# Performance work log

Hardware: AMD Instinct MI355X
Metric: run time of the kernel (lower is better)

Reference implementation:

```python
import jax, jax.numpy as jnp
import numpy as np

HEADS = 16
DIM_HEAD = 64
SCALE = DIM_HEAD ** -0.5
MASK_NEG = 1000000.0


def setup_inputs() -> dict:
    key = jax.random.key(0)
    ks = jax.random.split(key, 6)
    B, N, M, D = 2, 2048, 2048, 1024
    inner = HEADS * DIM_HEAD  # 1024
    x = jax.random.normal(ks[0], (B, N, D), dtype=jnp.float32)
    context = jax.random.normal(ks[1], (B, M, D), dtype=jnp.float32)
    mask = jax.random.randint(ks[2], (B, N), 0, 2, dtype=jnp.int32)
    Wq = jax.random.normal(ks[3], (D, inner), dtype=jnp.float32) * (D ** -0.5)
    Wkv = jax.random.normal(ks[4], (D, 2 * inner), dtype=jnp.float32) * (D ** -0.5)
    Wout = jax.random.normal(ks[5], (inner, D), dtype=jnp.float32) * (inner ** -0.5)
    bout = jnp.zeros((D,), dtype=jnp.float32)
    return {"x": x, "context": context, "mask": mask,
            "Wq": Wq, "Wkv": Wkv, "Wout": Wout, "bout": bout}


def _split_heads(t):
    # [b, n, (h d)] -> [b, h, n, d]
    b, n, _ = t.shape
    return t.reshape(b, n, HEADS, DIM_HEAD).transpose(0, 2, 1, 3)


def reference(x, context, mask, Wq, Wkv, Wout, bout):
    kv = context @ Wkv                      # [b, m, 2*inner]
    k, v = jnp.split(kv, 2, axis=-1)
    q = x @ Wq                              # [b, n, inner]
    q, k, v = _split_heads(q), _split_heads(k), _split_heads(v)
    dots = jnp.einsum('bhnd,bhmd->bhnm', q, k) * SCALE
    # mask is [b, n]: additive penalty per query row (faithful to source)
    dots = dots - (1.0 - mask.astype(jnp.float32))[:, None, :, None] * MASK_NEG
    attn = jax.nn.softmax(dots, axis=-1)
    out = jnp.einsum('bhnm,bhmd->bhnd', attn, v)  # [b, h, n, d]
    b, h, n, d = out.shape
    out = out.transpose(0, 2, 1, 3).reshape(b, n, h * d)
    return out @ Wout + bout
```

## Files before the change

kernel.cpp:

```cpp
#include <hip/hip_runtime.h>
#include <hip/hip_bf16.h>
#include <math.h>

#define BATCH   2
#define NQ      2048
#define NKV     2048
#define DMODEL  1024
#define HEADS   16
#define INNER   1024
#define KVCOLS  2048

typedef short bf16x8 __attribute__((ext_vector_type(8)));
typedef float f32x4  __attribute__((ext_vector_type(4)));

__device__ __forceinline__ short f2bf(float x) {
    __hip_bfloat16 h = __float2bfloat16(x);
    return *reinterpret_cast<short*>(&h);
}
__device__ __forceinline__ float bf2f(short h) {
    unsigned int u = ((unsigned int)(unsigned short)h) << 16;
    float f;
    __builtin_memcpy(&f, &u, 4);
    return f;
}
__device__ __forceinline__ void gl_lds16(const void* g, void* l) {
    __builtin_amdgcn_global_load_lds(
        (const __attribute__((address_space(1))) unsigned int*)g,
        (__attribute__((address_space(3))) unsigned int*)l, 16, 0, 0);
}
__device__ __forceinline__ int sw(int row, int chunk) {
    return row * 64 + ((chunk ^ (row & 7)) << 3);
}

__device__ __forceinline__ void split_chunk(const float* __restrict__ in,
                                            short* __restrict__ hi,
                                            short* __restrict__ lo, int id)
{
    const int i = (id * 256 + (int)threadIdx.x) * 4;
    float4 v = *(const float4*)(in + i);
    short4 h, l;
    h.x = f2bf(v.x); l.x = f2bf(v.x - bf2f(h.x));
    h.y = f2bf(v.y); l.y = f2bf(v.y - bf2f(h.y));
    h.z = f2bf(v.z); l.z = f2bf(v.z - bf2f(h.z));
    h.w = f2bf(v.w); l.w = f2bf(v.w - bf2f(h.w));
    *(short4*)(hi + i) = h;
    *(short4*)(lo + i) = l;
}

__device__ __forceinline__ void tile_transpose_split(
    const float* __restrict__ W, short* __restrict__ Wth, short* __restrict__ Wtl,
    int Kd, int Nd, int bx, int by, int split)
{
    __shared__ float t[32][33];
    const int lx = threadIdx.x & 31, ly = threadIdx.x >> 5;
    #pragma unroll
    for (int j = 0; j < 4; ++j)
        t[ly + j * 8][lx] = W[(size_t)(by * 32 + ly + j * 8) * Nd + bx * 32 + lx];
    __syncthreads();
    #pragma unroll
    for (int j = 0; j < 4; ++j) {
        const float v = t[lx][ly + j * 8];
        const short h = f2bf(v);
        const size_t idx = (size_t)(bx * 32 + ly + j * 8) * Kd + by * 32 + lx;
        Wth[idx] = h;
        if (split) Wtl[idx] = f2bf(v - bf2f(h));
    }
}

__global__ __launch_bounds__(256)
void prep_all(const float* __restrict__ x, const float* __restrict__ ctx,
              const float* __restrict__ Wq, const float* __restrict__ Wkv,
              const float* __restrict__ Wout,
              short* __restrict__ xh, short* __restrict__ xl,
              short* __restrict__ ch, short* __restrict__ cl,
              short* __restrict__ WqTh, short* __restrict__ WqTl,
              short* __restrict__ WkvTh, short* __restrict__ WkvTl,
              short* __restrict__ WoutT)
{
    const int id = blockIdx.x;
    if (id < 4096) {
        split_chunk(x, xh, xl, id);
    } else if (id < 8192) {
        split_chunk(ctx, ch, cl, id - 4096);
    } else {
        const int r = id - 8192;
        if (r < 1024)
            tile_transpose_split(Wq, WqTh, WqTl, 1024, 1024, r & 31, r >> 5, 1);
        else if (r < 3072)
            tile_transpose_split(Wkv, WkvTh, WkvTl, 1024, 2048, (r - 1024) & 63, (r - 1024) >> 6, 1);
        else
            tile_transpose_split(Wout, WoutT, nullptr, 1024, 1024, (r - 3072) & 31, (r - 3072) >> 5, 0);
    }
}

__global__ __launch_bounds__(256)
void qkv_gemm(const short* __restrict__ xh, const short* __restrict__ xl,
              const short* __restrict__ ch, const short* __restrict__ cl,
              const short* __restrict__ WqTh, const short* __restrict__ WqTl,
              const short* __restrict__ WkvTh, const short* __restrict__ WkvTl,
              short* __restrict__ qhp, short* __restrict__ qlp,
              short* __restrict__ khp, short* __restrict__ klp,
              short* __restrict__ vp)
{
    __shared__ short Ash[128 * 32];
    __shared__ short Asl[128 * 32];
    __shared__ short Bsh[128 * 32];
    __shared__ short Bsl[128 * 32];

    const int tid = threadIdx.x;
    const int z = blockIdx.z;
    const int m0 = blockIdx.y * 128, n0 = blockIdx.x * 128;
    const int w = tid >> 6, ln = tid & 63;
    const int wm = (w & 1) * 64, wn = (w >> 1) * 64;
    const int lr = ln & 15, lq = ln >> 4;
    const int terms = (z == 2) ? 1 : 3;

    const short* Ah  = (z == 0) ? xh : ch;
    const short* Al  = (z == 0) ? xl : cl;
    const short* Bth = (z == 0) ? WqTh : (z == 1 ? WkvTh : WkvTh + (size_t)1024 * 1024);
    const short* Btl = (z == 0) ? WqTl : WkvTl;

    f32x4 acc[4][4];
    #pragma unroll
    for (int mt = 0; mt < 4; ++mt)
        #pragma unroll
        for (int nt = 0; nt < 4; ++nt)
            #pragma unroll
            for (int r = 0; r < 4; ++r) acc[mt][nt][r] = 0.0f;

    for (int k0 = 0; k0 < 1024; k0 += 32) {
        __syncthreads();
        #pragma unroll
        for (int it = 0; it < 2; ++it) {
            const int f = it * 256 + tid;
            const int row = f >> 2, c = f & 3;
            const int cg = c ^ ((row >> 1) & 3);
            const size_t ao = (size_t)(m0 + row) * 1024 + k0 + cg * 8;
            const size_t bo = (size_t)(n0 + row) * 1024 + k0 + cg * 8;
            gl_lds16(Ah  + ao, Ash + f * 8);
            gl_lds16(Bth + bo, Bsh + f * 8);
            if (terms == 3) {
                gl_lds16(Al  + ao, Asl + f * 8);
                gl_lds16(Btl + bo, Bsl + f * 8);
            }
        }
        __syncthreads();

        bf16x8 ah[4], bh[4];
        #pragma unroll
        for (int t = 0; t < 4; ++t) {
            const int ar = wm + t * 16 + lr;
            const int br = wn + t * 16 + lr;
            ah[t] = *(const bf16x8*)(Ash + ar * 32 + ((lq ^ ((ar >> 1) & 3)) << 3));
            bh[t] = *(const bf16x8*)(Bsh + br * 32 + ((lq ^ ((br >> 1) & 3)) << 3));
        }
        #pragma unroll
        for (int mt = 0; mt < 4; ++mt)
            #pragma unroll
            for (int nt = 0; nt < 4; ++nt)
                acc[mt][nt] = __builtin_amdgcn_mfma_f32_16x16x32_bf16(
                    ah[mt], bh[nt], acc[mt][nt], 0, 0, 0);

        if (terms == 3) {
            bf16x8 al[4], bl[4];
            #pragma unroll
            for (int t = 0; t < 4; ++t) {
                const int ar = wm + t * 16 + lr;
                const int br = wn + t * 16 + lr;
                al[t] = *(const bf16x8*)(Asl + ar * 32 + ((lq ^ ((ar >> 1) & 3)) << 3));
                bl[t] = *(const bf16x8*)(Bsl + br * 32 + ((lq ^ ((br >> 1) & 3)) << 3));
            }
            #pragma unroll
            for (int mt = 0; mt < 4; ++mt)
                #pragma unroll
                for (int nt = 0; nt < 4; ++nt) {
                    acc[mt][nt] = __builtin_amdgcn_mfma_f32_16x16x32_bf16(
                        ah[mt], bl[nt], acc[mt][nt], 0, 0, 0);
                    acc[mt][nt] = __builtin_amdgcn_mfma_f32_16x16x32_bf16(
                        al[mt], bh[nt], acc[mt][nt], 0, 0, 0);
                }
        }
    }

    const float scale = (z == 0) ? 0.125f : 1.0f;
    short* Chi = (z == 0) ? qhp : (z == 1 ? khp : vp);
    short* Clo = (z == 0) ? qlp : klp;
    #pragma unroll
    for (int mt = 0; mt < 4; ++mt)
        #pragma unroll
        for (int nt = 0; nt < 4; ++nt)
            #pragma unroll
            for (int r = 0; r < 4; ++r) {
                const int row = m0 + wm + mt * 16 + lq * 4 + r;
                const int col = n0 + wn + nt * 16 + lr;
                const float v = acc[mt][nt][r] * scale;
                const short hh = f2bf(v);
                Chi[(size_t)row * 1024 + col] = hh;
                if (z != 2)
                    Clo[(size_t)row * 1024 + col] = f2bf(v - bf2f(hh));
            }
}

__global__ __launch_bounds__(256)
void gemm_out(const short* __restrict__ A, const short* __restrict__ Bt,
              float* __restrict__ C, int Md, int Nd, int Kd,
              const float* __restrict__ bias)
{
    __shared__ short As[64 * 64];
    __shared__ short Bs[64 * 64];
    const int tid = threadIdx.x;
    const int m0 = blockIdx.y * 64, n0 = blockIdx.x * 64;
    const int w = tid >> 6, ln = tid & 63;
    const int wm = (w & 1) * 32, wn = (w >> 1) * 32;
    const int lr = ln & 15, lq = ln >> 4;

    f32x4 acc[2][2];
    #pragma unroll
    for (int mt = 0; mt < 2; ++mt)
        #pragma unroll
        for (int nt = 0; nt < 2; ++nt)
            #pragma unroll
            for (int r = 0; r < 4; ++r) acc[mt][nt][r] = 0.0f;

    for (int k0 = 0; k0 < Kd; k0 += 64) {
        __syncthreads();
        #pragma unroll
        for (int it = 0; it < 2; ++it) {
            const int f = it * 256 + tid;
            const int row = f >> 3, c8 = f & 7;
            gl_lds16(A  + (size_t)(m0 + row) * Kd + k0 + c8 * 8, As + f * 8);
            gl_lds16(Bt + (size_t)(n0 + row) * Kd + k0 + c8 * 8, Bs + f * 8);
        }
        __syncthreads();
        #pragma unroll
        for (int ks = 0; ks < 2; ++ks) {
            bf16x8 af[2], bfr[2];
            #pragma unroll
            for (int t = 0; t < 2; ++t) {
                af[t]  = *(const bf16x8*)(As + (wm + t * 16 + lr) * 64 + ks * 32 + lq * 8);
                bfr[t] = *(const bf16x8*)(Bs + (wn + t * 16 + lr) * 64 + ks * 32 + lq * 8);
            }
            #pragma unroll
            for (int mt = 0; mt < 2; ++mt)
                #pragma unroll
                for (int nt = 0; nt < 2; ++nt)
                    acc[mt][nt] = __builtin_amdgcn_mfma_f32_16x16x32_bf16(
                        af[mt], bfr[nt], acc[mt][nt], 0, 0, 0);
        }
    }
    #pragma unroll
    for (int mt = 0; mt < 2; ++mt)
        #pragma unroll
        for (int nt = 0; nt < 2; ++nt)
            #pragma unroll
            for (int r = 0; r < 4; ++r) {
                const int row = m0 + wm + mt * 16 + lq * 4 + r;
                const int col = n0 + wn + nt * 16 + lr;
                C[(size_t)row * Nd + col] = acc[mt][nt][r] + bias[col];
            }
}

__global__ __launch_bounds__(512, 4)
void flash_v5(const short* __restrict__ qh, const short* __restrict__ ql,
              const short* __restrict__ kh, const short* __restrict__ kl,
              const short* __restrict__ vp, const int* __restrict__ mask,
              short* __restrict__ aob)
{
    const int qt = blockIdx.x, h = blockIdx.y, b = blockIdx.z;
    const int tid = threadIdx.x;
    const int w = tid >> 6, ln = tid & 63;
    const int lr = ln & 15, lq = ln >> 4;

    __shared__ short Kh[2 * 4096];
    __shared__ short Kl[2 * 4096];
    __shared__ short Vt[2 * 4096];
    __shared__ short Ps[128 * 64];

    const size_t qrow0 = (size_t)(b * NQ + qt * 128);

    bf16x8 aqh[2], aql[2];
    #pragma unroll
    for (int ks = 0; ks < 2; ++ks) {
        const size_t qoff = (qrow0 + w * 16 + lr) * INNER + h * 64 + ks * 32 + lq * 8;
        aqh[ks] = *(const bf16x8*)(qh + qoff);
        aql[ks] = *(const bf16x8*)(ql + qoff);
    }
    float keep[4];
    #pragma unroll
    for (int r = 0; r < 4; ++r)
        keep[r] = (float)mask[b * NQ + qt * 128 + w * 16 + lq * 4 + r];

    const int srow = tid >> 3, sc8 = tid & 7;
    const int kdst = sw(srow, sc8);
    const int kp = tid & 31, dg4 = (tid >> 5) * 4;
    int4 rkh, rkl; int2 rva, rvb;

    {
        const size_t koff = (size_t)(b * NKV + srow) * INNER + h * 64 + sc8 * 8;
        rkh = *(const int4*)(kh + koff);
        rkl = *(const int4*)(kl + koff);
        const short* v0 = vp + (size_t)(b * NKV + 2 * kp) * INNER + h * 64 + dg4;
        rva = *(const int2*)(v0);
        rvb = *(const int2*)(v0 + INNER);
        *(int4*)(Kh + kdst) = rkh;
        *(int4*)(Kl + kdst) = rkl;
        const short* as = (const short*)&rva;
        const short* bs = (const short*)&rvb;
        int* vt32 = (int*)Vt;
        #pragma unroll
        for (int j = 0; j < 4; ++j)
            vt32[(dg4 + j) * 32 + (((kp >> 2) ^ ((dg4 + j) & 7)) << 2) + (kp & 3)] =
                (int)((unsigned short)as[j] | ((unsigned int)(unsigned short)bs[j] << 16));
    }

    float psum[4];
    #pragma unroll
    for (int r = 0; r < 4; ++r) psum[r] = 0.0f;
    f32x4 oacc[4];
    #pragma unroll
    for (int dg = 0; dg < 4; ++dg)
        #pragma unroll
        for (int r = 0; r < 4; ++r) oacc[dg][r] = 0.0f;

    for (int kt = 0; kt < NKV / 64; ++kt) {
        const int cur = kt & 1;
        if (kt < NKV / 64 - 1) {
            const size_t krow0 = (size_t)(b * NKV + (kt + 1) * 64);
            const size_t koff = (krow0 + srow) * INNER + h * 64 + sc8 * 8;
            rkh = *(const int4*)(kh + koff);
            rkl = *(const int4*)(kl + koff);
            const short* v0 = vp + (krow0 + 2 * kp) * INNER + h * 64 + dg4;
            rva = *(const int2*)(v0);
            rvb = *(const int2*)(v0 + INNER);
        }
        __syncthreads();

        const short* KhC = Kh + cur * 4096;
        const short* KlC = Kl + cur * 4096;
        const short* VtC = Vt + cur * 4096;

        f32x4 sacc[4];
        #pragma unroll
        for (int g = 0; g < 4; ++g)
            #pragma unroll
            for (int r = 0; r < 4; ++r) sacc[g][r] = 0.0f;
        #pragma unroll
        for (int ks = 0; ks < 2; ++ks) {
            #pragma unroll
            for (int g = 0; g < 4; ++g) {
                const bf16x8 bkh = *(const bf16x8*)(KhC + sw(g * 16 + lr, ks * 4 + lq));
                const bf16x8 bkl = *(const bf16x8*)(KlC + sw(g * 16 + lr, ks * 4 + lq));
                sacc[g] = __builtin_amdgcn_mfma_f32_16x16x32_bf16(aqh[ks], bkh, sacc[g], 0, 0, 0);
                sacc[g] = __builtin_amdgcn_mfma_f32_16x16x32_bf16(aqh[ks], bkl, sacc[g], 0, 0, 0);
                sacc[g] = __builtin_amdgcn_mfma_f32_16x16x32_bf16(aql[ks], bkh, sacc[g], 0, 0, 0);
            }
        }

        #pragma unroll
        for (int r = 0; r < 4; ++r) {
            const int prow = w * 16 + lq * 4 + r;
            #pragma unroll
            for (int g = 0; g < 4; ++g) {
                float s = sacc[g][r];
                if (keep[r] == 0.0f) s = rintf(s * 16.0f) * 0.0625f;
                const float p = __expf(s);
                psum[r] += p;
                Ps[sw(prow, g * 2 + (lr >> 3)) + (lr & 7)] = f2bf(p);
            }
        }

        #pragma unroll
        for (int ks = 0; ks < 2; ++ks) {
            const bf16x8 ap = *(const bf16x8*)(Ps + sw(w * 16 + lr, ks * 4 + lq));
            #pragma unroll
            for (int dg = 0; dg < 4; ++dg) {
                const bf16x8 bv = *(const bf16x8*)(VtC + sw(dg * 16 + lr, ks * 4 + lq));
                oacc[dg] = __builtin_amdgcn_mfma_f32_16x16x32_bf16(ap, bv, oacc[dg], 0, 0, 0);
            }
        }

        if (kt < NKV / 64 - 1) {
            short* KhN = Kh + (cur ^ 1) * 4096;
            short* KlN = Kl + (cur ^ 1) * 4096;
            *(int4*)(KhN + kdst) = rkh;
            *(int4*)(KlN + kdst) = rkl;
            const short* as = (const short*)&rva;
            const short* bs = (const short*)&rvb;
            int* vt32 = (int*)(Vt + (cur ^ 1) * 4096);
            #pragma unroll
            for (int j = 0; j < 4; ++j)
                vt32[(dg4 + j) * 32 + (((kp >> 2) ^ ((dg4 + j) & 7)) << 2) + (kp & 3)] =
                    (int)((unsigned short)as[j] | ((unsigned int)(unsigned short)bs[j] << 16));
        }
    }

    #pragma unroll
    for (int off = 1; off < 16; off <<= 1)
        #pragma unroll
        for (int r = 0; r < 4; ++r)
            psum[r] += __shfl_xor(psum[r], off, 64);

    #pragma unroll
    for (int dg = 0; dg < 4; ++dg)
        #pragma unroll
        for (int r = 0; r < 4; ++r) {
            const int row = w * 16 + lq * 4 + r;
            aob[(qrow0 + row) * INNER + h * 64 + dg * 16 + lr] =
                f2bf(oacc[dg][r] / psum[r]);
        }
}

extern "C" void kernel_launch(void* const* d_in, const int* in_sizes, int n_in,
                              void* d_out, int out_size, void* d_ws, size_t ws_size,
                              hipStream_t stream)
{
    const float* x    = (const float*)d_in[0];
    const float* ctx  = (const float*)d_in[1];
    const int*   mask = (const int*)d_in[2];
    const float* Wq   = (const float*)d_in[3];
    const float* Wkv  = (const float*)d_in[4];
    const float* Wout = (const float*)d_in[5];
    const float* bout = (const float*)d_in[6];
    float* out = (float*)d_out;

    short* base  = (short*)d_ws;
    short* xh    = base;
    short* xl    = base + (size_t)4 * 1024 * 1024;
    short* aob   = xh;
    short* WqTh  = base + (size_t) 8 * 1024 * 1024;
    short* WqTl  = base + (size_t) 9 * 1024 * 1024;
    short* qhp   = base + (size_t)10 * 1024 * 1024;
    short* qlp   = base + (size_t)14 * 1024 * 1024;
    short* WkvTh = base + (size_t)18 * 1024 * 1024;
    short* WkvTl = base + (size_t)20 * 1024 * 1024;
    short* khp   = base + (size_t)22 * 1024 * 1024;
    short* klp   = base + (size_t)26 * 1024 * 1024;
    short* WoutT = base + (size_t)30 * 1024 * 1024;
    short* ch    = base + (size_t)31 * 1024 * 1024;
    short* cl    = base + (size_t)35 * 1024 * 1024;
    short* vp    = base + (size_t)39 * 1024 * 1024;

    const dim3 blk(256);
    prep_all<<<12288, blk, 0, stream>>>(x, ctx, Wq, Wkv, Wout,
                                        xh, xl, ch, cl,
                                        WqTh, WqTl, WkvTh, WkvTl, WoutT);
    qkv_gemm<<<dim3(8, 32, 3), blk, 0, stream>>>(
        xh, xl, ch, cl, WqTh, WqTl, WkvTh, WkvTl,
        qhp, qlp, khp, klp, vp);
    flash_v5<<<dim3(NQ / 128, HEADS, BATCH), dim3(512), 0, stream>>>(
        qhp, qlp, khp, klp, vp, mask, aob);
    gemm_out<<<dim3(1024 / 64, 4096 / 64), blk, 0, stream>>>(
        aob, WoutT, out, 4096, 1024, 1024, bout);
}
```

Before: 281.2 us.

## Read A operands directly from global in GEMMs, widen K tile, permute P/V layouts

Both GEMMs stop staging the A operand in LDS: each wave loads its activation fragments straight from global memory into registers, and only the weight operand goes through LDS, which now uses an XOR swizzle over eight column groups. The QKV GEMM doubles its K step to 64, and the output GEMM grows to 128-row tiles with hard-coded dimensions. In the attention kernel, each lane now writes its four P values as one short4, and the K index mapping for the V^T staging is permuted to match the new P column order. The aim is to cut LDS traffic, barriers and store instructions. The cost is uncoalesced, cache-dependent global loads for A, issued right before the MFMAs with no prefetch to hide their latency.

```diff
diff --git a/kernel.cpp b/kernel.cpp
--- a/kernel.cpp
+++ b/kernel.cpp
@@ -102,10 +102,8 @@
               short* __restrict__ khp, short* __restrict__ klp,
               short* __restrict__ vp)
 {
-    __shared__ short Ash[128 * 32];
-    __shared__ short Asl[128 * 32];
-    __shared__ short Bsh[128 * 32];
-    __shared__ short Bsl[128 * 32];
+    __shared__ short Bsh[128 * 64];
+    __shared__ short Bsl[128 * 64];
 
     const int tid = threadIdx.x;
     const int z = blockIdx.z;
@@ -128,57 +126,53 @@
             #pragma unroll
             for (int r = 0; r < 4; ++r) acc[mt][nt][r] = 0.0f;
 
-    for (int k0 = 0; k0 < 1024; k0 += 32) {
+    for (int k0 = 0; k0 < 1024; k0 += 64) {
         __syncthreads();
         #pragma unroll
-        for (int it = 0; it < 2; ++it) {
+        for (int it = 0; it < 4; ++it) {
             const int f = it * 256 + tid;
-            const int row = f >> 2, c = f & 3;
-            const int cg = c ^ ((row >> 1) & 3);
-            const size_t ao = (size_t)(m0 + row) * 1024 + k0 + cg * 8;
+            const int row = f >> 3, c8 = f & 7;
+            const int cg = c8 ^ (row & 7);
             const size_t bo = (size_t)(n0 + row) * 1024 + k0 + cg * 8;
-            gl_lds16(Ah  + ao, Ash + f * 8);
             gl_lds16(Bth + bo, Bsh + f * 8);
-            if (terms == 3) {
-                gl_lds16(Al  + ao, Asl + f * 8);
-                gl_lds16(Btl + bo, Bsl + f * 8);
-            }
+            if (terms == 3) gl_lds16(Btl + bo, Bsl + f * 8);
         }
         __syncthreads();
 
-        bf16x8 ah[4], bh[4];
-        #pragma unroll
-        for (int t = 0; t < 4; ++t) {
-            const int ar = wm + t * 16 + lr;
-            const int br = wn + t * 16 + lr;
-            ah[t] = *(const bf16x8*)(Ash + ar * 32 + ((lq ^ ((ar >> 1) & 3)) << 3));
-            bh[t] = *(const bf16x8*)(Bsh + br * 32 + ((lq ^ ((br >> 1) & 3)) << 3));
-        }
-        #pragma unroll
-        for (int mt = 0; mt < 4; ++mt)
-            #pragma unroll
-            for (int nt = 0; nt < 4; ++nt)
-                acc[mt][nt] = __builtin_amdgcn_mfma_f32_16x16x32_bf16(
-                    ah[mt], bh[nt], acc[mt][nt], 0, 0, 0);
-
-        if (terms == 3) {
-            bf16x8 al[4], bl[4];
+        #pragma unroll
+        for (int ks = 0; ks < 2; ++ks) {
+            bf16x8 ah[4], al[4];
             #pragma unroll
             for (int t = 0; t < 4; ++t) {
-                const int ar = wm + t * 16 + lr;
+                const size_t ao = (size_t)(m0 + wm + t * 16 + lr) * 1024 + k0 + ks * 32 + lq * 8;
+                ah[t] = *(const bf16x8*)(Ah + ao);
+                if (terms == 3) al[t] = *(const bf16x8*)(Al + ao);
+            }
+            bf16x8 bh[4], bl[4];
+            #pragma unroll
+            for (int t = 0; t < 4; ++t) {
                 const int br = wn + t * 16 + lr;
-                al[t] = *(const bf16x8*)(Asl + ar * 32 + ((lq ^ ((ar >> 1) & 3)) << 3));
-                bl[t] = *(const bf16x8*)(Bsl + br * 32 + ((lq ^ ((br >> 1) & 3)) << 3));
+                const int pc = (ks * 4 + lq) ^ (br & 7);
+                bh[t] = *(const bf16x8*)(Bsh + br * 64 + (pc << 3));
+                if (terms == 3) bl[t] = *(const bf16x8*)(Bsl + br * 64 + (pc << 3));
             }
             #pragma unroll
             for (int mt = 0; mt < 4; ++mt)
                 #pragma unroll
-                for (int nt = 0; nt < 4; ++nt) {
+                for (int nt = 0; nt < 4; ++nt)
                     acc[mt][nt] = __builtin_amdgcn_mfma_f32_16x16x32_bf16(
-                        ah[mt], bl[nt], acc[mt][nt], 0, 0, 0);
-                    acc[mt][nt] = __builtin_amdgcn_mfma_f32_16x16x32_bf16(
-                        al[mt], bh[nt], acc[mt][nt], 0, 0, 0);
-                }
+                        ah[mt], bh[nt], acc[mt][nt], 0, 0, 0);
+            if (terms == 3) {
+                #pragma unroll
+                for (int mt = 0; mt < 4; ++mt)
+                    #pragma unroll
+                    for (int nt = 0; nt < 4; ++nt) {
+                        acc[mt][nt] = __builtin_amdgcn_mfma_f32_16x16x32_bf16(
+                            ah[mt], bl[nt], acc[mt][nt], 0, 0, 0);
+                        acc[mt][nt] = __builtin_amdgcn_mfma_f32_16x16x32_bf16(
+                            al[mt], bh[nt], acc[mt][nt], 0, 0, 0);
+                    }
+            }
         }
     }
 
@@ -203,45 +197,47 @@
 
 __global__ __launch_bounds__(256)
 void gemm_out(const short* __restrict__ A, const short* __restrict__ Bt,
-              float* __restrict__ C, int Md, int Nd, int Kd,
-              const float* __restrict__ bias)
-{
-    __shared__ short As[64 * 64];
+              float* __restrict__ C, const float* __restrict__ bias)
+{
     __shared__ short Bs[64 * 64];
     const int tid = threadIdx.x;
-    const int m0 = blockIdx.y * 64, n0 = blockIdx.x * 64;
+    const int m0 = blockIdx.y * 128, n0 = blockIdx.x * 64;
     const int w = tid >> 6, ln = tid & 63;
-    const int wm = (w & 1) * 32, wn = (w >> 1) * 32;
+    const int wm = (w & 1) * 64, wn = (w >> 1) * 32;
     const int lr = ln & 15, lq = ln >> 4;
 
-    f32x4 acc[2][2];
-    #pragma unroll
-    for (int mt = 0; mt < 2; ++mt)
+    f32x4 acc[4][2];
+    #pragma unroll
+    for (int mt = 0; mt < 4; ++mt)
         #pragma unroll
         for (int nt = 0; nt < 2; ++nt)
             #pragma unroll
             for (int r = 0; r < 4; ++r) acc[mt][nt][r] = 0.0f;
 
-    for (int k0 = 0; k0 < Kd; k0 += 64) {
+    for (int k0 = 0; k0 < 1024; k0 += 64) {
         __syncthreads();
         #pragma unroll
         for (int it = 0; it < 2; ++it) {
             const int f = it * 256 + tid;
             const int row = f >> 3, c8 = f & 7;
-            gl_lds16(A  + (size_t)(m0 + row) * Kd + k0 + c8 * 8, As + f * 8);
-            gl_lds16(Bt + (size_t)(n0 + row) * Kd + k0 + c8 * 8, Bs + f * 8);
+            const int cg = c8 ^ (row & 7);
+            gl_lds16(Bt + (size_t)(n0 + row) * 1024 + k0 + cg * 8, Bs + f * 8);
         }
         __syncthreads();
         #pragma unroll
         for (int ks = 0; ks < 2; ++ks) {
-            bf16x8 af[2], bfr[2];
+            bf16x8 af[4], bfr[2];
+            #pragma unroll
+            for (int t = 0; t < 4; ++t)
+                af[t] = *(const bf16x8*)(A + (size_t)(m0 + wm + t * 16 + lr) * 1024
+                                         + k0 + ks * 32 + lq * 8);
             #pragma unroll
             for (int t = 0; t < 2; ++t) {
-                af[t]  = *(const bf16x8*)(As + (wm + t * 16 + lr) * 64 + ks * 32 + lq * 8);
-                bfr[t] = *(const bf16x8*)(Bs + (wn + t * 16 + lr) * 64 + ks * 32 + lq * 8);
-            }
-            #pragma unroll
-            for (int mt = 0; mt < 2; ++mt)
+                const int br = wn + t * 16 + lr;
+                bfr[t] = *(const bf16x8*)(Bs + br * 64 + (((ks * 4 + lq) ^ (br & 7)) << 3));
+            }
+            #pragma unroll
+            for (int mt = 0; mt < 4; ++mt)
                 #pragma unroll
                 for (int nt = 0; nt < 2; ++nt)
                     acc[mt][nt] = __builtin_amdgcn_mfma_f32_16x16x32_bf16(
@@ -249,19 +245,19 @@
         }
     }
     #pragma unroll
-    for (int mt = 0; mt < 2; ++mt)
+    for (int mt = 0; mt < 4; ++mt)
         #pragma unroll
         for (int nt = 0; nt < 2; ++nt)
             #pragma unroll
             for (int r = 0; r < 4; ++r) {
                 const int row = m0 + wm + mt * 16 + lq * 4 + r;
                 const int col = n0 + wn + nt * 16 + lr;
-                C[(size_t)row * Nd + col] = acc[mt][nt][r] + bias[col];
+                C[(size_t)row * 1024 + col] = acc[mt][nt][r] + bias[col];
             }
 }
 
 __global__ __launch_bounds__(512, 4)
-void flash_v5(const short* __restrict__ qh, const short* __restrict__ ql,
+void flash_v6(const short* __restrict__ qh, const short* __restrict__ ql,
               const short* __restrict__ kh, const short* __restrict__ kl,
               const short* __restrict__ vp, const int* __restrict__ mask,
               short* __restrict__ aob)
@@ -292,16 +288,18 @@
 
     const int srow = tid >> 3, sc8 = tid & 7;
     const int kdst = sw(srow, sc8);
-    const int kp = tid & 31, dg4 = (tid >> 5) * 4;
+    const int idx = tid & 31, dg4 = (tid >> 5) * 4;
+    const int vj  = (idx & 15) + ((idx >> 4) << 5);
+    const int kp32 = (idx & 15) * 2 + (idx >> 4);
     int4 rkh, rkl; int2 rva, rvb;
 
     {
         const size_t koff = (size_t)(b * NKV + srow) * INNER + h * 64 + sc8 * 8;
         rkh = *(const int4*)(kh + koff);
         rkl = *(const int4*)(kl + koff);
-        const short* v0 = vp + (size_t)(b * NKV + 2 * kp) * INNER + h * 64 + dg4;
+        const short* v0 = vp + (size_t)(b * NKV + vj) * INNER + h * 64 + dg4;
         rva = *(const int2*)(v0);
-        rvb = *(const int2*)(v0 + INNER);
+        rvb = *(const int2*)(v0 + 16 * INNER);
         *(int4*)(Kh + kdst) = rkh;
         *(int4*)(Kl + kdst) = rkl;
         const short* as = (const short*)&rva;
@@ -309,7 +307,7 @@
         int* vt32 = (int*)Vt;
         #pragma unroll
         for (int j = 0; j < 4; ++j)
-            vt32[(dg4 + j) * 32 + (((kp >> 2) ^ ((dg4 + j) & 7)) << 2) + (kp & 3)] =
+            vt32[(dg4 + j) * 32 + (((kp32 >> 2) ^ ((dg4 + j) & 7)) << 2) + (kp32 & 3)] =
                 (int)((unsigned short)as[j] | ((unsigned int)(unsigned short)bs[j] << 16));
     }
 
@@ -329,9 +327,9 @@
             const size_t koff = (krow0 + srow) * INNER + h * 64 + sc8 * 8;
             rkh = *(const int4*)(kh + koff);
             rkl = *(const int4*)(kl + koff);
-            const short* v0 = vp + (krow0 + 2 * kp) * INNER + h * 64 + dg4;
+            const short* v0 = vp + (krow0 + vj) * INNER + h * 64 + dg4;
             rva = *(const int2*)(v0);
-            rvb = *(const int2*)(v0 + INNER);
+            rvb = *(const int2*)(v0 + 16 * INNER);
         }
         __syncthreads();
 
@@ -359,14 +357,18 @@
         #pragma unroll
         for (int r = 0; r < 4; ++r) {
             const int prow = w * 16 + lq * 4 + r;
+            float pv[4];
             #pragma unroll
             for (int g = 0; g < 4; ++g) {
                 float s = sacc[g][r];
                 if (keep[r] == 0.0f) s = rintf(s * 16.0f) * 0.0625f;
-                const float p = __expf(s);
-                psum[r] += p;
-                Ps[sw(prow, g * 2 + (lr >> 3)) + (lr & 7)] = f2bf(p);
-            }
+                pv[g] = __expf(s);
+                psum[r] += pv[g];
+            }
+            short4 pw;
+            pw.x = f2bf(pv[0]); pw.y = f2bf(pv[1]);
+            pw.z = f2bf(pv[2]); pw.w = f2bf(pv[3]);
+            *(short4*)(Ps + sw(prow, lr >> 1) + (lr & 1) * 4) = pw;
         }
 
         #pragma unroll
@@ -389,7 +391,7 @@
             int* vt32 = (int*)(Vt + (cur ^ 1) * 4096);
             #pragma unroll
             for (int j = 0; j < 4; ++j)
-                vt32[(dg4 + j) * 32 + (((kp >> 2) ^ ((dg4 + j) & 7)) << 2) + (kp & 3)] =
+                vt32[(dg4 + j) * 32 + (((kp32 >> 2) ^ ((dg4 + j) & 7)) << 2) + (kp32 & 3)] =
                     (int)((unsigned short)as[j] | ((unsigned int)(unsigned short)bs[j] << 16));
         }
     }
@@ -447,8 +449,8 @@
     qkv_gemm<<<dim3(8, 32, 3), blk, 0, stream>>>(
         xh, xl, ch, cl, WqTh, WqTl, WkvTh, WkvTl,
         qhp, qlp, khp, klp, vp);
-    flash_v5<<<dim3(NQ / 128, HEADS, BATCH), dim3(512), 0, stream>>>(
+    flash_v6<<<dim3(NQ / 128, HEADS, BATCH), dim3(512), 0, stream>>>(
         qhp, qlp, khp, klp, vp, mask, aob);
-    gemm_out<<<dim3(1024 / 64, 4096 / 64), blk, 0, stream>>>(
-        aob, WoutT, out, 4096, 1024, 1024, bout);
-}
+    gemm_out<<<dim3(1024 / 64, 4096 / 128), blk, 0, stream>>>(
+        aob, WoutT, out, bout);
+}
```

After: 323.2 us. 14.9% more time.

## Double-buffer QKV GEMM LDS tiles and vectorize flash P stores

Applied to the files above, without the earlier changes.

The QKV GEMM replaces direct global-to-LDS loads with register prefetch of the next K slice into a second LDS buffer, so global loads overlap the MFMA work and one barrier per iteration can be dropped. Its swizzle changes from (row>>1)&3 to row&3. In the flash kernel, the V transpose loads are remapped so each thread pairs rows 16 apart, and the P tile is permuted to match. This lets each thread write its four probabilities as one short4 LDS store instead of four scalar stores. The cost is double the GEMM LDS footprint and more registers held for prefetch, which may lower occupancy.

```diff
diff --git a/kernel.cpp b/kernel.cpp
--- a/kernel.cpp
+++ b/kernel.cpp
@@ -102,10 +102,10 @@
               short* __restrict__ khp, short* __restrict__ klp,
               short* __restrict__ vp)
 {
-    __shared__ short Ash[128 * 32];
-    __shared__ short Asl[128 * 32];
-    __shared__ short Bsh[128 * 32];
-    __shared__ short Bsl[128 * 32];
+    __shared__ short Ash[2][128 * 32];
+    __shared__ short Asl[2][128 * 32];
+    __shared__ short Bsh[2][128 * 32];
+    __shared__ short Bsl[2][128 * 32];
 
     const int tid = threadIdx.x;
     const int z = blockIdx.z;
@@ -120,6 +120,12 @@
     const short* Bth = (z == 0) ? WqTh : (z == 1 ? WkvTh : WkvTh + (size_t)1024 * 1024);
     const short* Btl = (z == 0) ? WqTl : WkvTl;
 
+    const int f0r = tid >> 2,         f0c = tid & 3;
+    const int f1r = (256 + tid) >> 2, f1c = tid & 3;
+    const int g0 = f0c ^ (f0r & 3), g1 = f1c ^ (f1r & 3);
+
+    int4 pah[2], pal[2], pbh[2], pbl[2];
+
     f32x4 acc[4][4];
     #pragma unroll
     for (int mt = 0; mt < 4; ++mt)
@@ -128,20 +134,40 @@
             #pragma unroll
             for (int r = 0; r < 4; ++r) acc[mt][nt][r] = 0.0f;
 
-    for (int k0 = 0; k0 < 1024; k0 += 32) {
-        __syncthreads();
-        #pragma unroll
-        for (int it = 0; it < 2; ++it) {
-            const int f = it * 256 + tid;
-            const int row = f >> 2, c = f & 3;
-            const int cg = c ^ ((row >> 1) & 3);
-            const size_t ao = (size_t)(m0 + row) * 1024 + k0 + cg * 8;
-            const size_t bo = (size_t)(n0 + row) * 1024 + k0 + cg * 8;
-            gl_lds16(Ah  + ao, Ash + f * 8);
-            gl_lds16(Bth + bo, Bsh + f * 8);
+    {
+        const size_t a0 = (size_t)(m0 + f0r) * 1024 + g0 * 8;
+        const size_t a1 = (size_t)(m0 + f1r) * 1024 + g1 * 8;
+        const size_t b0 = (size_t)(n0 + f0r) * 1024 + g0 * 8;
+        const size_t b1 = (size_t)(n0 + f1r) * 1024 + g1 * 8;
+        pah[0] = *(const int4*)(Ah + a0);  pah[1] = *(const int4*)(Ah + a1);
+        pbh[0] = *(const int4*)(Bth + b0); pbh[1] = *(const int4*)(Bth + b1);
+        *(int4*)(&Ash[0][tid * 8])         = pah[0];
+        *(int4*)(&Ash[0][(256 + tid) * 8]) = pah[1];
+        *(int4*)(&Bsh[0][tid * 8])         = pbh[0];
+        *(int4*)(&Bsh[0][(256 + tid) * 8]) = pbh[1];
+        if (terms == 3) {
+            pal[0] = *(const int4*)(Al + a0);  pal[1] = *(const int4*)(Al + a1);
+            pbl[0] = *(const int4*)(Btl + b0); pbl[1] = *(const int4*)(Btl + b1);
+            *(int4*)(&Asl[0][tid * 8])         = pal[0];
+            *(int4*)(&Asl[0][(256 + tid) * 8]) = pal[1];
+            *(int4*)(&Bsl[0][tid * 8])         = pbl[0];
+            *(int4*)(&Bsl[0][(256 + tid) * 8]) = pbl[1];
+        }
+    }
+
+    for (int kt = 0; kt < 32; ++kt) {
+        const int cur = kt & 1;
+        if (kt < 31) {
+            const int k0 = (kt + 1) * 32;
+            const size_t a0 = (size_t)(m0 + f0r) * 1024 + k0 + g0 * 8;
+            const size_t a1 = (size_t)(m0 + f1r) * 1024 + k0 + g1 * 8;
+            const size_t b0 = (size_t)(n0 + f0r) * 1024 + k0 + g0 * 8;
+            const size_t b1 = (size_t)(n0 + f1r) * 1024 + k0 + g1 * 8;
+            pah[0] = *(const int4*)(Ah + a0);  pah[1] = *(const int4*)(Ah + a1);
+            pbh[0] = *(const int4*)(Bth + b0); pbh[1] = *(const int4*)(Bth + b1);
             if (terms == 3) {
-                gl_lds16(Al  + ao, Asl + f * 8);
-                gl_lds16(Btl + bo, Bsl + f * 8);
+                pal[0] = *(const int4*)(Al + a0);  pal[1] = *(const int4*)(Al + a1);
+                pbl[0] = *(const int4*)(Btl + b0); pbl[1] = *(const int4*)(Btl + b1);
             }
         }
         __syncthreads();
@@ -151,8 +177,8 @@
         for (int t = 0; t < 4; ++t) {
             const int ar = wm + t * 16 + lr;
             const int br = wn + t * 16 + lr;
-            ah[t] = *(const bf16x8*)(Ash + ar * 32 + ((lq ^ ((ar >> 1) & 3)) << 3));
-            bh[t] = *(const bf16x8*)(Bsh + br * 32 + ((lq ^ ((br >> 1) & 3)) << 3));
+            ah[t] = *(const bf16x8*)(&Ash[cur][ar * 32 + ((lq ^ (ar & 3)) << 3)]);
+            bh[t] = *(const bf16x8*)(&Bsh[cur][br * 32 + ((lq ^ (br & 3)) << 3)]);
         }
         #pragma unroll
         for (int mt = 0; mt < 4; ++mt)
@@ -160,15 +186,14 @@
             for (int nt = 0; nt < 4; ++nt)
                 acc[mt][nt] = __builtin_amdgcn_mfma_f32_16x16x32_bf16(
                     ah[mt], bh[nt], acc[mt][nt], 0, 0, 0);
-
         if (terms == 3) {
             bf16x8 al[4], bl[4];
             #pragma unroll
             for (int t = 0; t < 4; ++t) {
                 const int ar = wm + t * 16 + lr;
                 const int br = wn + t * 16 + lr;
-                al[t] = *(const bf16x8*)(Asl + ar * 32 + ((lq ^ ((ar >> 1) & 3)) << 3));
-                bl[t] = *(const bf16x8*)(Bsl + br * 32 + ((lq ^ ((br >> 1) & 3)) << 3));
+                al[t] = *(const bf16x8*)(&Asl[cur][ar * 32 + ((lq ^ (ar & 3)) << 3)]);
+                bl[t] = *(const bf16x8*)(&Bsl[cur][br * 32 + ((lq ^ (br & 3)) << 3)]);
             }
             #pragma unroll
             for (int mt = 0; mt < 4; ++mt)
@@ -180,6 +205,20 @@
                         al[mt], bh[nt], acc[mt][nt], 0, 0, 0);
                 }
         }
+
+        if (kt < 31) {
+            const int nb = cur ^ 1;
+            *(int4*)(&Ash[nb][tid * 8])         = pah[0];
+            *(int4*)(&Ash[nb][(256 + tid) * 8]) = pah[1];
+            *(int4*)(&Bsh[nb][tid * 8])         = pbh[0];
+            *(int4*)(&Bsh[nb][(256 + tid) * 8]) = pbh[1];
+            if (terms == 3) {
+                *(int4*)(&Asl[nb][tid * 8])         = pal[0];
+                *(int4*)(&Asl[nb][(256 + tid) * 8]) = pal[1];
+                *(int4*)(&Bsl[nb][tid * 8])         = pbl[0];
+                *(int4*)(&Bsl[nb][(256 + tid) * 8]) = pbl[1];
+            }
+        }
     }
 
     const float scale = (z == 0) ? 0.125f : 1.0f;
@@ -261,7 +300,7 @@
 }
 
 __global__ __launch_bounds__(512, 4)
-void flash_v5(const short* __restrict__ qh, const short* __restrict__ ql,
+void flash_v6(const short* __restrict__ qh, const short* __restrict__ ql,
               const short* __restrict__ kh, const short* __restrict__ kl,
               const short* __restrict__ vp, const int* __restrict__ mask,
               short* __restrict__ aob)
@@ -292,16 +331,18 @@
 
     const int srow = tid >> 3, sc8 = tid & 7;
     const int kdst = sw(srow, sc8);
-    const int kp = tid & 31, dg4 = (tid >> 5) * 4;
+    const int idx = tid & 31, dg4 = (tid >> 5) * 4;
+    const int vj  = (idx & 15) + ((idx >> 4) << 5);
+    const int kp32 = (idx & 15) * 2 + (idx >> 4);
     int4 rkh, rkl; int2 rva, rvb;
 
     {
         const size_t koff = (size_t)(b * NKV + srow) * INNER + h * 64 + sc8 * 8;
         rkh = *(const int4*)(kh + koff);
         rkl = *(const int4*)(kl + koff);
-        const short* v0 = vp + (size_t)(b * NKV + 2 * kp) * INNER + h * 64 + dg4;
+        const short* v0 = vp + (size_t)(b * NKV + vj) * INNER + h * 64 + dg4;
         rva = *(const int2*)(v0);
-        rvb = *(const int2*)(v0 + INNER);
+        rvb = *(const int2*)(v0 + 16 * INNER);
         *(int4*)(Kh + kdst) = rkh;
         *(int4*)(Kl + kdst) = rkl;
         const short* as = (const short*)&rva;
@@ -309,7 +350,7 @@
         int* vt32 = (int*)Vt;
         #pragma unroll
         for (int j = 0; j < 4; ++j)
-            vt32[(dg4 + j) * 32 + (((kp >> 2) ^ ((dg4 + j) & 7)) << 2) + (kp & 3)] =
+            vt32[(dg4 + j) * 32 + (((kp32 >> 2) ^ ((dg4 + j) & 7)) << 2) + (kp32 & 3)] =
                 (int)((unsigned short)as[j] | ((unsigned int)(unsigned short)bs[j] << 16));
     }
 
@@ -329,9 +370,9 @@
             const size_t koff = (krow0 + srow) * INNER + h * 64 + sc8 * 8;
             rkh = *(const int4*)(kh + koff);
             rkl = *(const int4*)(kl + koff);
-            const short* v0 = vp + (krow0 + 2 * kp) * INNER + h * 64 + dg4;
+            const short* v0 = vp + (krow0 + vj) * INNER + h * 64 + dg4;
             rva = *(const int2*)(v0);
-            rvb = *(const int2*)(v0 + INNER);
+            rvb = *(const int2*)(v0 + 16 * INNER);
         }
         __syncthreads();
 
@@ -359,14 +400,18 @@
         #pragma unroll
         for (int r = 0; r < 4; ++r) {
             const int prow = w * 16 + lq * 4 + r;
+            float pv[4];
             #pragma unroll
             for (int g = 0; g < 4; ++g) {
                 float s = sacc[g][r];
                 if (keep[r] == 0.0f) s = rintf(s * 16.0f) * 0.0625f;
-                const float p = __expf(s);
-                psum[r] += p;
-                Ps[sw(prow, g * 2 + (lr >> 3)) + (lr & 7)] = f2bf(p);
-            }
+                pv[g] = __expf(s);
+                psum[r] += pv[g];
+            }
+            short4 pw;
+            pw.x = f2bf(pv[0]); pw.y = f2bf(pv[1]);
+            pw.z = f2bf(pv[2]); pw.w = f2bf(pv[3]);
+            *(short4*)(Ps + sw(prow, lr >> 1) + (lr & 1) * 4) = pw;
         }
 
         #pragma unroll
@@ -389,7 +434,7 @@
             int* vt32 = (int*)(Vt + (cur ^ 1) * 4096);
             #pragma unroll
             for (int j = 0; j < 4; ++j)
-                vt32[(dg4 + j) * 32 + (((kp >> 2) ^ ((dg4 + j) & 7)) << 2) + (kp & 3)] =
+                vt32[(dg4 + j) * 32 + (((kp32 >> 2) ^ ((dg4 + j) & 7)) << 2) + (kp32 & 3)] =
                     (int)((unsigned short)as[j] | ((unsigned int)(unsigned short)bs[j] << 16));
         }
     }
@@ -447,7 +492,7 @@
     qkv_gemm<<<dim3(8, 32, 3), blk, 0, stream>>>(
         xh, xl, ch, cl, WqTh, WqTl, WkvTh, WkvTl,
         qhp, qlp, khp, klp, vp);
-    flash_v5<<<dim3(NQ / 128, HEADS, BATCH), dim3(512), 0, stream>>>(
+    flash_v6<<<dim3(NQ / 128, HEADS, BATCH), dim3(512), 0, stream>>>(
         qhp, qlp, khp, klp, vp, mask, aob);
     gemm_out<<<dim3(1024 / 64, 4096 / 64), blk, 0, stream>>>(
         aob, WoutT, out, 4096, 1024, 1024, bout);
```

Result: slower. 377.9 us (+34.4%).

## Halve flash block to 4 waves, each computing two 16-row query tiles

Applied to the files above, without the earlier changes.

The attention kernel drops from 8 waves to 4 waves per 128-row query block. Each wave now owns 32 query rows as two MFMA row tiles, so every K and V fragment read from LDS feeds twice as many MFMAs. Global-to-LDS staging now has each thread load two K rows and wider V chunks, and the P tile is written to LDS as packed 4-element stores instead of scalar stores. This cuts LDS read traffic per MFMA but raises register pressure and lowers the number of waves available to hide latency.

```diff
diff --git a/kernel.cpp b/kernel.cpp
--- a/kernel.cpp
+++ b/kernel.cpp
@@ -260,8 +260,8 @@
             }
 }
 
-__global__ __launch_bounds__(512, 4)
-void flash_v5(const short* __restrict__ qh, const short* __restrict__ ql,
+__global__ __launch_bounds__(256, 2)
+void flash_v7(const short* __restrict__ qh, const short* __restrict__ ql,
               const short* __restrict__ kh, const short* __restrict__ kl,
               const short* __restrict__ vp, const int* __restrict__ mask,
               short* __restrict__ aob)
@@ -278,60 +278,73 @@
 
     const size_t qrow0 = (size_t)(b * NQ + qt * 128);
 
-    bf16x8 aqh[2], aql[2];
-    #pragma unroll
-    for (int ks = 0; ks < 2; ++ks) {
-        const size_t qoff = (qrow0 + w * 16 + lr) * INNER + h * 64 + ks * 32 + lq * 8;
-        aqh[ks] = *(const bf16x8*)(qh + qoff);
-        aql[ks] = *(const bf16x8*)(ql + qoff);
-    }
-    float keep[4];
-    #pragma unroll
-    for (int r = 0; r < 4; ++r)
-        keep[r] = (float)mask[b * NQ + qt * 128 + w * 16 + lq * 4 + r];
+    bf16x8 aqh[2][2], aql[2][2];
+    #pragma unroll
+    for (int mt = 0; mt < 2; ++mt)
+        #pragma unroll
+        for (int ks = 0; ks < 2; ++ks) {
+            const size_t qoff = (qrow0 + w * 32 + mt * 16 + lr) * INNER
+                              + h * 64 + ks * 32 + lq * 8;
+            aqh[mt][ks] = *(const bf16x8*)(qh + qoff);
+            aql[mt][ks] = *(const bf16x8*)(ql + qoff);
+        }
+    float keep[2][4];
+    #pragma unroll
+    for (int mt = 0; mt < 2; ++mt)
+        #pragma unroll
+        for (int r = 0; r < 4; ++r)
+            keep[mt][r] = (float)mask[b * NQ + qt * 128 + w * 32 + mt * 16 + lq * 4 + r];
 
     const int srow = tid >> 3, sc8 = tid & 7;
-    const int kdst = sw(srow, sc8);
-    const int kp = tid & 31, dg4 = (tid >> 5) * 4;
-    int4 rkh, rkl; int2 rva, rvb;
+    const int kdst0 = sw(srow, sc8), kdst1 = sw(32 + srow, sc8);
+    const int idx = tid & 31, dg8 = (tid >> 5) * 8;
+    const int vj  = (idx & 15) + ((idx >> 4) << 5);
+    const int kp32 = (idx & 15) * 2 + (idx >> 4);
+    int4 rkh[2], rkl[2], rva, rvb;
 
     {
-        const size_t koff = (size_t)(b * NKV + srow) * INNER + h * 64 + sc8 * 8;
-        rkh = *(const int4*)(kh + koff);
-        rkl = *(const int4*)(kl + koff);
-        const short* v0 = vp + (size_t)(b * NKV + 2 * kp) * INNER + h * 64 + dg4;
-        rva = *(const int2*)(v0);
-        rvb = *(const int2*)(v0 + INNER);
-        *(int4*)(Kh + kdst) = rkh;
-        *(int4*)(Kl + kdst) = rkl;
+        const size_t koff0 = (size_t)(b * NKV + srow) * INNER + h * 64 + sc8 * 8;
+        const size_t koff1 = (size_t)(b * NKV + 32 + srow) * INNER + h * 64 + sc8 * 8;
+        rkh[0] = *(const int4*)(kh + koff0); rkh[1] = *(const int4*)(kh + koff1);
+        rkl[0] = *(const int4*)(kl + koff0); rkl[1] = *(const int4*)(kl + koff1);
+        const short* v0 = vp + (size_t)(b * NKV + vj) * INNER + h * 64 + dg8;
+        rva = *(const int4*)(v0);
+        rvb = *(const int4*)(v0 + 16 * INNER);
+        *(int4*)(Kh + kdst0) = rkh[0]; *(int4*)(Kh + kdst1) = rkh[1];
+        *(int4*)(Kl + kdst0) = rkl[0]; *(int4*)(Kl + kdst1) = rkl[1];
         const short* as = (const short*)&rva;
         const short* bs = (const short*)&rvb;
         int* vt32 = (int*)Vt;
         #pragma unroll
-        for (int j = 0; j < 4; ++j)
-            vt32[(dg4 + j) * 32 + (((kp >> 2) ^ ((dg4 + j) & 7)) << 2) + (kp & 3)] =
+        for (int j = 0; j < 8; ++j)
+            vt32[(dg8 + j) * 32 + (((kp32 >> 2) ^ ((dg8 + j) & 7)) << 2) + (kp32 & 3)] =
                 (int)((unsigned short)as[j] | ((unsigned int)(unsigned short)bs[j] << 16));
     }
 
-    float psum[4];
-    #pragma unroll
-    for (int r = 0; r < 4; ++r) psum[r] = 0.0f;
-    f32x4 oacc[4];
-    #pragma unroll
-    for (int dg = 0; dg < 4; ++dg)
-        #pragma unroll
-        for (int r = 0; r < 4; ++r) oacc[dg][r] = 0.0f;
+    float psum[2][4];
+    #pragma unroll
+    for (int mt = 0; mt < 2; ++mt)
+        #pragma unroll
+        for (int r = 0; r < 4; ++r) psum[mt][r] = 0.0f;
+    f32x4 oacc[2][4];
+    #pragma unroll
+    for (int mt = 0; mt < 2; ++mt)
+        #pragma unroll
+        for (int dg = 0; dg < 4; ++dg)
+            #pragma unroll
+            for (int r = 0; r < 4; ++r) oacc[mt][dg][r] = 0.0f;
 
     for (int kt = 0; kt < NKV / 64; ++kt) {
         const int cur = kt & 1;
         if (kt < NKV / 64 - 1) {
             const size_t krow0 = (size_t)(b * NKV + (kt + 1) * 64);
-            const size_t koff = (krow0 + srow) * INNER + h * 64 + sc8 * 8;
-            rkh = *(const int4*)(kh + koff);
-            rkl = *(const int4*)(kl + koff);
-            const short* v0 = vp + (krow0 + 2 * kp) * INNER + h * 64 + dg4;
-            rva = *(const int2*)(v0);
-            rvb = *(const int2*)(v0 + INNER);
+            const size_t koff0 = (krow0 + srow) * INNER + h * 64 + sc8 * 8;
+            const size_t koff1 = (krow0 + 32 + srow) * INNER + h * 64 + sc8 * 8;
+            rkh[0] = *(const int4*)(kh + koff0); rkh[1] = *(const int4*)(kh + koff1);
+            rkl[0] = *(const int4*)(kl + koff0); rkl[1] = *(const int4*)(kl + koff1);
+            const short* v0 = vp + (krow0 + vj) * INNER + h * 64 + dg8;
+            rva = *(const int4*)(v0);
+            rvb = *(const int4*)(v0 + 16 * INNER);
         }
         __syncthreads();
 
@@ -339,57 +352,77 @@
         const short* KlC = Kl + cur * 4096;
         const short* VtC = Vt + cur * 4096;
 
-        f32x4 sacc[4];
-        #pragma unroll
-        for (int g = 0; g < 4; ++g)
-            #pragma unroll
-            for (int r = 0; r < 4; ++r) sacc[g][r] = 0.0f;
+        f32x4 sacc[2][4];
+        #pragma unroll
+        for (int mt = 0; mt < 2; ++mt)
+            #pragma unroll
+            for (int g = 0; g < 4; ++g)
+                #pragma unroll
+                for (int r = 0; r < 4; ++r) sacc[mt][g][r] = 0.0f;
         #pragma unroll
         for (int ks = 0; ks < 2; ++ks) {
             #pragma unroll
             for (int g = 0; g < 4; ++g) {
                 const bf16x8 bkh = *(const bf16x8*)(KhC + sw(g * 16 + lr, ks * 4 + lq));
                 const bf16x8 bkl = *(const bf16x8*)(KlC + sw(g * 16 + lr, ks * 4 + lq));
-                sacc[g] = __builtin_amdgcn_mfma_f32_16x16x32_bf16(aqh[ks], bkh, sacc[g], 0, 0, 0);
-                sacc[g] = __builtin_amdgcn_mfma_f32_16x16x32_bf16(aqh[ks], bkl, sacc[g], 0, 0, 0);
-                sacc[g] = __builtin_amdgcn_mfma_f32_16x16x32_bf16(aql[ks], bkh, sacc[g], 0, 0, 0);
-            }
-        }
-
-        #pragma unroll
-        for (int r = 0; r < 4; ++r) {
-            const int prow = w * 16 + lq * 4 + r;
-            #pragma unroll
-            for (int g = 0; g < 4; ++g) {
-                float s = sacc[g][r];
-                if (keep[r] == 0.0f) s = rintf(s * 16.0f) * 0.0625f;
-                const float p = __expf(s);
-                psum[r] += p;
-                Ps[sw(prow, g * 2 + (lr >> 3)) + (lr & 7)] = f2bf(p);
-            }
-        }
+                #pragma unroll
+                for (int mt = 0; mt < 2; ++mt) {
+                    sacc[mt][g] = __builtin_amdgcn_mfma_f32_16x16x32_bf16(
+                        aqh[mt][ks], bkh, sacc[mt][g], 0, 0, 0);
+                    sacc[mt][g] = __builtin_amdgcn_mfma_f32_16x16x32_bf16(
+                        aqh[mt][ks], bkl, sacc[mt][g], 0, 0, 0);
+                    sacc[mt][g] = __builtin_amdgcn_mfma_f32_16x16x32_bf16(
+                        aql[mt][ks], bkh, sacc[mt][g], 0, 0, 0);
+                }
+            }
+        }
+
+        #pragma unroll
+        for (int mt = 0; mt < 2; ++mt)
+            #pragma unroll
+            for (int r = 0; r < 4; ++r) {
+                const int prow = w * 32 + mt * 16 + lq * 4 + r;
+                float pv[4];
+                #pragma unroll
+                for (int g = 0; g < 4; ++g) {
+                    float s = sacc[mt][g][r];
+                    if (keep[mt][r] == 0.0f) s = rintf(s * 16.0f) * 0.0625f;
+                    pv[g] = __expf(s);
+                    psum[mt][r] += pv[g];
+                }
+                short4 pw;
+                pw.x = f2bf(pv[0]); pw.y = f2bf(pv[1]);
+                pw.z = f2bf(pv[2]); pw.w = f2bf(pv[3]);
+                *(short4*)(Ps + sw(prow, lr >> 1) + (lr & 1) * 4) = pw;
+            }
 
         #pragma unroll
         for (int ks = 0; ks < 2; ++ks) {
-            const bf16x8 ap = *(const bf16x8*)(Ps + sw(w * 16 + lr, ks * 4 + lq));
+            bf16x8 ap[2];
+            #pragma unroll
+            for (int mt = 0; mt < 2; ++mt)
+                ap[mt] = *(const bf16x8*)(Ps + sw(w * 32 + mt * 16 + lr, ks * 4 + lq));
             #pragma unroll
             for (int dg = 0; dg < 4; ++dg) {
                 const bf16x8 bv = *(const bf16x8*)(VtC + sw(dg * 16 + lr, ks * 4 + lq));
-                oacc[dg] = __builtin_amdgcn_mfma_f32_16x16x32_bf16(ap, bv, oacc[dg], 0, 0, 0);
+                #pragma unroll
+                for (int mt = 0; mt < 2; ++mt)
+                    oacc[mt][dg] = __builtin_amdgcn_mfma_f32_16x16x32_bf16(
+                        ap[mt], bv, oacc[mt][dg], 0, 0, 0);
             }
         }
 
         if (kt < NKV / 64 - 1) {
             short* KhN = Kh + (cur ^ 1) * 4096;
             short* KlN = Kl + (cur ^ 1) * 4096;
-            *(int4*)(KhN + kdst) = rkh;
-            *(int4*)(KlN + kdst) = rkl;
+            *(int4*)(KhN + kdst0) = rkh[0]; *(int4*)(KhN + kdst1) = rkh[1];
+            *(int4*)(KlN + kdst0) = rkl[0]; *(int4*)(KlN + kdst1) = rkl[1];
             const short* as = (const short*)&rva;
             const short* bs = (const short*)&rvb;
             int* vt32 = (int*)(Vt + (cur ^ 1) * 4096);
             #pragma unroll
-            for (int j = 0; j < 4; ++j)
-                vt32[(dg4 + j) * 32 + (((kp >> 2) ^ ((dg4 + j) & 7)) << 2) + (kp & 3)] =
+            for (int j = 0; j < 8; ++j)
+                vt32[(dg8 + j) * 32 + (((kp32 >> 2) ^ ((dg8 + j) & 7)) << 2) + (kp32 & 3)] =
                     (int)((unsigned short)as[j] | ((unsigned int)(unsigned short)bs[j] << 16));
         }
     }
@@ -397,17 +430,21 @@
     #pragma unroll
     for (int off = 1; off < 16; off <<= 1)
         #pragma unroll
-        for (int r = 0; r < 4; ++r)
-            psum[r] += __shfl_xor(psum[r], off, 64);
-
-    #pragma unroll
-    for (int dg = 0; dg < 4; ++dg)
-        #pragma unroll
-        for (int r = 0; r < 4; ++r) {
-            const int row = w * 16 + lq * 4 + r;
-            aob[(qrow0 + row) * INNER + h * 64 + dg * 16 + lr] =
-                f2bf(oacc[dg][r] / psum[r]);
-        }
+        for (int mt = 0; mt < 2; ++mt)
+            #pragma unroll
+            for (int r = 0; r < 4; ++r)
+                psum[mt][r] += __shfl_xor(psum[mt][r], off, 64);
+
+    #pragma unroll
+    for (int mt = 0; mt < 2; ++mt)
+        #pragma unroll
+        for (int dg = 0; dg < 4; ++dg)
+            #pragma unroll
+            for (int r = 0; r < 4; ++r) {
+                const int row = w * 32 + mt * 16 + lq * 4 + r;
+                aob[(qrow0 + row) * INNER + h * 64 + dg * 16 + lr] =
+                    f2bf(oacc[mt][dg][r] / psum[mt][r]);
+            }
 }
 
 extern "C" void kernel_launch(void* const* d_in, const int* in_sizes, int n_in,
@@ -447,7 +484,7 @@
     qkv_gemm<<<dim3(8, 32, 3), blk, 0, stream>>>(
         xh, xl, ch, cl, WqTh, WqTl, WkvTh, WkvTl,
         qhp, qlp, khp, klp, vp);
-    flash_v5<<<dim3(NQ / 128, HEADS, BATCH), dim3(512), 0, stream>>>(
+    flash_v7<<<dim3(NQ / 128, HEADS, BATCH), blk, 0, stream>>>(
         qhp, qlp, khp, klp, vp, mask, aob);
     gemm_out<<<dim3(1024 / 64, 4096 / 64), blk, 0, stream>>>(
         aob, WoutT, out, 4096, 1024, 1024, bout);
```

After: 299.1 us. 6.4% more time.
